# Kernel optimization log

Measured on AMD Instinct MI355X. Metric: run time of the kernel, lower is better.

## Reference

```python
import jax, jax.numpy as jnp
import numpy as np

NUM_HEADS = 8
LN_EPS = 1e-5


def setup_inputs() -> dict:
    key = jax.random.key(0)
    ks = jax.random.split(key, 8)
    B, C1, C2, H, W, D = 8, 384, 192, 16, 16, 16
    A = C1  # all_head_size = num_heads * (C1 // num_heads)
    s1, s2, sA = 1.0 / np.sqrt(C1), 1.0 / np.sqrt(C2), 1.0 / np.sqrt(A)
    return {
        "x1": jax.random.normal(ks[0], (B, C1, H, W, D), jnp.float32),
        "x2": jax.random.normal(ks[1], (B, C2, H, W, D), jnp.float32),
        "Wq": jax.random.normal(ks[2], (C1, A), jnp.float32) * s1,
        "bq": jnp.zeros((A,), jnp.float32),
        "Wk": jax.random.normal(ks[3], (C2, A), jnp.float32) * s2,
        "bk": jnp.zeros((A,), jnp.float32),
        "Wv": jax.random.normal(ks[4], (C2, A), jnp.float32) * s2,
        "bv": jnp.zeros((A,), jnp.float32),
        "Wo": jax.random.normal(ks[5], (A, C1), jnp.float32) * sA,
        "bo": jnp.zeros((C1,), jnp.float32),
        "gamma": jnp.ones((C1,), jnp.float32),
        "beta": jnp.zeros((C1,), jnp.float32),
    }


def reference(x1, x2, Wq, bq, Wk, bk, Wv, bv, Wo, bo, gamma, beta):
    B, C1, H, W, D = x1.shape
    L = H * W * D
    nh = NUM_HEADS
    dh = C1 // nh
    # flatten spatial dims to tokens: [B, L, C]
    x1f = x1.reshape(B, C1, L).transpose(0, 2, 1)
    x2f = x2.reshape(B, x2.shape[1], L).transpose(0, 2, 1)
    scale = dh ** 0.25
    q = (x1f @ Wq + bq).reshape(B, L, nh, dh) / scale  # [B,L,h,d]
    k = (x2f @ Wk + bk).reshape(B, L, nh, dh) / scale
    v = (x2f @ Wv + bv).reshape(B, L, nh, dh)
    # softmax over the token (L) axis of keys
    ksm = jax.nn.softmax(k, axis=1)
    # kernelized attention: KV outer product [B,h,d,e], then Q . KV
    kv = jnp.einsum('blhd,blhe->bhde', ksm, v)
    ctx = jnp.einsum('blhd,bhde->blhe', q, kv).reshape(B, L, nh * dh)
    out = ctx @ Wo + bo + x1f  # residual
    # LayerNorm over channel dim
    mu = out.mean(axis=-1, keepdims=True)
    var = out.var(axis=-1, keepdims=True)
    out = (out - mu) * jax.lax.rsqrt(var + LN_EPS) * gamma + beta
    return out.transpose(0, 2, 1).reshape(B, C1, H, W, D)
```

## Files before the change

kernel.cpp:

```cpp
#include <hip/hip_runtime.h>
#include <hip/hip_bf16.h>
#include <math.h>

#define BB 8
#define C1D 384
#define C2D 192
#define LDIM 4096
#define ADIM 384
#define NH 8
#define DHD 48
#define KVLC 16
#define KVP_STRIDE 2352
#define LN_EPS 1e-5f

typedef short s8v __attribute__((ext_vector_type(8)));
typedef float f4v __attribute__((ext_vector_type(4)));

__device__ __forceinline__ unsigned short f2bf(float f) {
    unsigned u = __builtin_bit_cast(unsigned, f);
    unsigned r = (u + 0x7FFFu + ((u >> 16) & 1u)) >> 16;
    return (unsigned short)r;
}
__device__ __forceinline__ float bf2f(unsigned short h) {
    unsigned u = ((unsigned)h) << 16;
    return __builtin_bit_cast(float, u);
}
__device__ __forceinline__ void gload16(const void* g, void* l) {
    __builtin_amdgcn_global_load_lds((const __attribute__((address_space(1))) void*)g,
                                     (__attribute__((address_space(3))) void*)l, 16, 0, 0);
}

__device__ __forceinline__ void tcvt_body(const float* __restrict__ ib,
                                          unsigned short* __restrict__ ob,
                                          int R, int Cols, int c0, int r0,
                                          float* smem, int t)
{
#pragma unroll
    for (int i = 0; i < 4; ++i) {
        int idx = t + i * 256;
        int rr = idx >> 5, cc = idx & 31;
        smem[rr * 33 + cc] = ib[(size_t)(r0 + rr) * Cols + c0 + cc];
    }
    __syncthreads();
#pragma unroll
    for (int i = 0; i < 2; ++i) {
        int idx = t + i * 256;
        int cc = idx >> 4, rp = (idx & 15) * 2;
        unsigned val = (unsigned)f2bf(smem[rp * 33 + cc]) | ((unsigned)f2bf(smem[(rp + 1) * 33 + cc]) << 16);
        *(unsigned*)&ob[(size_t)(c0 + cc) * R + r0 + rp] = val;
    }
}

__global__ __launch_bounds__(256) void pack_all(
    const float* __restrict__ x1, const float* __restrict__ x2,
    const float* __restrict__ Wk, const float* __restrict__ Wv, const float* __restrict__ Wo,
    const float* __restrict__ bk, const float* __restrict__ bv,
    unsigned short* __restrict__ X1p, unsigned short* __restrict__ X2p,
    unsigned short* __restrict__ Wkvp, unsigned short* __restrict__ WoTp,
    float* __restrict__ bkv)
{
    __shared__ float smem[32 * 33];
    int bid = blockIdx.x;
    int t = threadIdx.x;
    if (bid < 12288) {
        int i = bid;
        int c0 = (i % 128) * 32, r0 = ((i / 128) % 12) * 32, b = i / 1536;
        tcvt_body(x1 + (size_t)b * C1D * LDIM, X1p + (size_t)b * C1D * LDIM,
                  C1D, LDIM, c0, r0, smem, t);
    } else if (bid < 18432) {
        int i = bid - 12288;
        int c0 = (i % 128) * 32, r0 = ((i / 128) % 6) * 32, b = i / 768;
        tcvt_body(x2 + (size_t)b * C2D * LDIM, X2p + (size_t)b * C2D * LDIM,
                  C2D, LDIM, c0, r0, smem, t);
    } else if (bid < 18720) {
        int i = bid - 18432;
        if (i < 72)       tcvt_body(Wk, Wkvp,                      C2D,  ADIM, (i % 12) * 32, (i / 12) * 32, smem, t);
        else if (i < 144) { i -= 72;  tcvt_body(Wv, Wkvp + (size_t)ADIM * C2D, C2D, ADIM, (i % 12) * 32, (i / 12) * 32, smem, t); }
        else              { i -= 144; tcvt_body(Wo, WoTp,          ADIM, C1D,  (i % 12) * 32, (i / 12) * 32, smem, t); }
    } else {
        for (int i = t; i < 768; i += 256) bkv[i] = (i < 384) ? bk[i] : bv[i - 384];
    }
}

template<int KD, int BMODE>
__global__ __launch_bounds__(256) void gemm_mfma(
    const unsigned short* __restrict__ A, size_t Abs,
    const unsigned short* __restrict__ Bt, size_t Bbs,
    const float* __restrict__ bias,
    unsigned short* __restrict__ Out, size_t Obs, int Ncols,
    float scl, float scl2, int msplit, int gx, int gy)
{
    __shared__ unsigned short As[128 * 64];
    __shared__ unsigned short Bs[128 * 64];
    const int t = threadIdx.x;
    const int lane = t & 63;
    const int w = t >> 6;
    const int wm = w >> 1, wn = w & 1;
    const int nwg = gridDim.x;
    const int bid = blockIdx.x;
    const int swz = (bid & 7) * (nwg >> 3) + (bid >> 3);
    const int m0 = (swz % gx) * 128;
    const int n0 = ((swz / gx) % gy) * 128;
    const int b  = swz / (gx * gy);
    const float sEff = (m0 < msplit) ? scl : scl2;

    const unsigned short* Ab = A + Abs * b + (size_t)m0 * KD;
    const unsigned short* Bb = Bt + Bbs * b + (size_t)n0 * KD;

    f4v acc[4][4];
#pragma unroll
    for (int i = 0; i < 4; ++i)
#pragma unroll
        for (int j = 0; j < 4; ++j) acc[i][j] = (f4v)0.f;

    const int r_l = lane >> 3;
    const int q = lane & 7;

    for (int ks = 0; ks < KD; ks += 64) {
#pragma unroll
        for (int c = 0; c < 4; ++c) {
            int row = w * 32 + c * 8 + r_l;
            int koff = ((q ^ (row & 7)) << 3);
            gload16(Ab + (size_t)row * KD + ks + koff, &As[(w * 32 + c * 8) * 64]);
            gload16(Bb + (size_t)row * KD + ks + koff, &Bs[(w * 32 + c * 8) * 64]);
        }
        __syncthreads();
#pragma unroll
        for (int kh = 0; kh < 2; ++kh) {
            s8v af[4], bfr[4];
            int kq = kh * 4 + (lane >> 4);
#pragma unroll
            for (int m = 0; m < 4; ++m) {
                int row = wm * 64 + m * 16 + (lane & 15);
                af[m] = *(const s8v*)&As[row * 64 + ((kq ^ (row & 7)) << 3)];
            }
#pragma unroll
            for (int n = 0; n < 4; ++n) {
                int row = wn * 64 + n * 16 + (lane & 15);
                bfr[n] = *(const s8v*)&Bs[row * 64 + ((kq ^ (row & 7)) << 3)];
            }
#pragma unroll
            for (int m = 0; m < 4; ++m)
#pragma unroll
                for (int n = 0; n < 4; ++n)
                    acc[m][n] = __builtin_amdgcn_mfma_f32_16x16x32_bf16(af[m], bfr[n], acc[m][n], 0, 0, 0);
        }
        __syncthreads();
    }

    float bn[4], bm[4][4];
    if (BMODE == 2) {
#pragma unroll
        for (int m = 0; m < 4; ++m)
#pragma unroll
            for (int r = 0; r < 4; ++r)
                bm[m][r] = bias[m0 + wm * 64 + m * 16 + (lane >> 4) * 4 + r];
    } else if (BMODE == 1) {
#pragma unroll
        for (int n = 0; n < 4; ++n) bn[n] = bias[n0 + wn * 64 + n * 16 + (lane & 15)];
    }
#pragma unroll
    for (int m = 0; m < 4; ++m)
#pragma unroll
        for (int n = 0; n < 4; ++n) {
            int col = n0 + wn * 64 + n * 16 + (lane & 15);
#pragma unroll
            for (int r = 0; r < 4; ++r) {
                int row = m0 + wm * 64 + m * 16 + (lane >> 4) * 4 + r;
                float bb = (BMODE == 2) ? bm[m][r] : (BMODE == 1) ? bn[n] : 0.f;
                float v = (acc[m][n][r] + bb) * sEff;
                if (BMODE == 3 && row == col) v += 1.f;
                Out[Obs * b + (size_t)row * Ncols + col] = f2bf(v);
            }
        }
}

__global__ __launch_bounds__(64) void kv_part(const unsigned short* __restrict__ KVt,
                                              float* __restrict__ kvpart)
{
    int lane = threadIdx.x;
    int b = blockIdx.z, h = blockIdx.y, lc = blockIdx.x;
    size_t base = ((size_t)b * 768 + h * DHD) * LDIM;
    const unsigned short* Kb = KVt + base;
    const unsigned short* Vb = Kb + (size_t)ADIM * LDIM;
    int lbase = lc * (LDIM / KVLC);

    f4v acc[3][3];
#pragma unroll
    for (int i = 0; i < 3; ++i)
#pragma unroll
        for (int j = 0; j < 3; ++j) acc[i][j] = (f4v)0.f;
    float es[3] = {0.f, 0.f, 0.f};

    for (int ks = 0; ks < LDIM / KVLC; ks += 32) {
        int l0 = lbase + ks + ((lane >> 4) * 8);
        s8v af[3], bfr[3];
#pragma unroll
        for (int me = 0; me < 3; ++me)
            af[me] = *(const s8v*)&Vb[(size_t)(me * 16 + (lane & 15)) * LDIM + l0];
#pragma unroll
        for (int nd = 0; nd < 3; ++nd) {
            s8v raw = *(const s8v*)&Kb[(size_t)(nd * 16 + (lane & 15)) * LDIM + l0];
#pragma unroll
            for (int j = 0; j < 8; ++j) {
                float e = __expf(bf2f((unsigned short)raw[j]));
                es[nd] += e;
                bfr[nd][j] = (short)f2bf(e);
            }
        }
#pragma unroll
        for (int me = 0; me < 3; ++me)
#pragma unroll
            for (int nd = 0; nd < 3; ++nd)
                acc[me][nd] = __builtin_amdgcn_mfma_f32_16x16x32_bf16(af[me], bfr[nd], acc[me][nd], 0, 0, 0);
    }
    float* pp = kvpart + (((size_t)(b * NH + h) * KVLC) + lc) * KVP_STRIDE;
#pragma unroll
    for (int me = 0; me < 3; ++me)
#pragma unroll
        for (int nd = 0; nd < 3; ++nd)
#pragma unroll
            for (int r = 0; r < 4; ++r) {
                int e = me * 16 + (lane >> 4) * 4 + r;
                int d = nd * 16 + (lane & 15);
                pp[e * DHD + d] = acc[me][nd][r];
            }
#pragma unroll
    for (int nd = 0; nd < 3; ++nd) {
        float s = es[nd];
        s += __shfl_xor(s, 16, 64);
        s += __shfl_xor(s, 32, 64);
        if (lane < 16) pp[2304 + nd * 16 + lane] = s;
    }
}

__global__ __launch_bounds__(256) void kv_finalize(const float* __restrict__ kvpart,
                                                   float* __restrict__ KVf)
{
    __shared__ float isl_s[DHD];
    int bh = blockIdx.x, t = threadIdx.x;
    const float* pp = kvpart + (size_t)bh * KVLC * KVP_STRIDE;
    if (t < DHD) {
        float s = 0.f;
#pragma unroll
        for (int lc = 0; lc < KVLC; ++lc) s += pp[lc * KVP_STRIDE + 2304 + t];
        isl_s[t] = 1.f / s;
    }
    __syncthreads();
    for (int idx = t; idx < DHD * DHD; idx += 256) {
        int d = idx / DHD, e = idx % DHD;
        float s = 0.f;
#pragma unroll
        for (int lc = 0; lc < KVLC; ++lc) s += pp[lc * KVP_STRIDE + e * DHD + d];
        KVf[(size_t)bh * DHD * DHD + idx] = s * isl_s[d];
    }
}

__global__ __launch_bounds__(256) void mb_kernel(const float* __restrict__ Wq,
                                                 const float* __restrict__ bq,
                                                 const float* __restrict__ KVf,
                                                 const float* __restrict__ Wo,
                                                 const float* __restrict__ bo,
                                                 unsigned short* __restrict__ M,
                                                 float* __restrict__ btot, float inv_scale)
{
    __shared__ float smem[DHD * DHD];
    int blk = blockIdx.x, t = threadIdx.x;
    if (blk < 384) {
        int c0 = (blk % 6) * 64, h = (blk / 6) % 8, b = blk / 48;
        for (int idx = t; idx < DHD * DHD; idx += 256)
            smem[idx] = KVf[((size_t)(b * NH + h)) * DHD * DHD + idx];
        __syncthreads();
        int cl = t >> 2, qq = t & 3;
        int c = c0 + cl;
        float wq[DHD];
#pragma unroll
        for (int d = 0; d < DHD; ++d) wq[d] = Wq[(size_t)c * ADIM + h * DHD + d];
        float s[12];
#pragma unroll
        for (int j = 0; j < 12; ++j) s[j] = 0.f;
#pragma unroll
        for (int d = 0; d < DHD; ++d) {
            float w = wq[d];
#pragma unroll
            for (int j = 0; j < 12; ++j)
                s[j] += w * smem[d * DHD + qq * 12 + j];
        }
#pragma unroll
        for (int j = 0; j < 12; ++j)
            M[((size_t)b * C1D + c) * ADIM + h * DHD + qq * 12 + j] = f2bf(s[j] * inv_scale);
    } else {
        int k = blk - 384;
        int cp0 = (k % 12) * 32, b = k / 12;
        for (int idx = t; idx < ADIM; idx += 256) {
            int h = idx / DHD, e = idx % DHD;
            float s = 0.f;
#pragma unroll
            for (int d = 0; d < DHD; ++d)
                s += bq[h * DHD + d] * KVf[((size_t)(b * NH + h)) * DHD * DHD + d * DHD + e];
            smem[idx] = s * inv_scale;
        }
        __syncthreads();
        int cp = cp0 + (t >> 3), part = t & 7;
        float s = 0.f;
#pragma unroll
        for (int i = 0; i < 48; ++i) {
            int he = part * 48 + i;
            s += smem[he] * Wo[(size_t)he * C1D + cp];
        }
        s += __shfl_xor(s, 1, 64);
        s += __shfl_xor(s, 2, 64);
        s += __shfl_xor(s, 4, 64);
        if (part == 0) btot[b * C1D + cp] = s + bo[cp];
    }
}

__global__ __launch_bounds__(512) void gemm_lnT(
    const unsigned short* __restrict__ Wr,
    const unsigned short* __restrict__ Bx,
    const float* __restrict__ btot,
    const float* __restrict__ gamma,
    const float* __restrict__ beta,
    float* __restrict__ Y)
{
    __shared__ __align__(16) char lds[65536];
    unsigned short* As = (unsigned short*)lds;
    unsigned short* Bs = (unsigned short*)(lds + 49152);
    float* stats = (float*)lds;
    float* fin   = (float*)(lds + 8192);

    const int t = threadIdx.x;
    const int lane = t & 63;
    const int w = t >> 6;
    const int bid = blockIdx.x;
    const int swz = (bid & 7) * 32 + (bid >> 3);
    const int l0 = (swz & 31) * 128;
    const int b  = swz >> 5;

    const unsigned short* Ab = Wr + (size_t)b * C1D * C1D;
    const unsigned short* Bb = Bx + ((size_t)b * LDIM + l0) * C1D;

    f4v acc[3][8];
#pragma unroll
    for (int m = 0; m < 3; ++m)
#pragma unroll
        for (int n = 0; n < 8; ++n) acc[m][n] = (f4v)0.f;

    const int r_l = lane >> 3;
    const int q = lane & 7;

    for (int ks = 0; ks < C1D; ks += 64) {
#pragma unroll
        for (int c = 0; c < 6; ++c) {
            int row = w * 48 + c * 8 + r_l;
            int koff = ((q ^ (row & 7)) << 3);
            gload16(Ab + (size_t)row * C1D + ks + koff, &As[(w * 48 + c * 8) * 64]);
        }
#pragma unroll
        for (int c = 0; c < 2; ++c) {
            int row = w * 16 + c * 8 + r_l;
            int koff = ((q ^ (row & 7)) << 3);
            gload16(Bb + (size_t)row * C1D + ks + koff, &Bs[(w * 16 + c * 8) * 64]);
        }
        __syncthreads();
#pragma unroll
        for (int kh = 0; kh < 2; ++kh) {
            int kq = kh * 4 + (lane >> 4);
            s8v af[3], bfr[8];
#pragma unroll
            for (int m = 0; m < 3; ++m) {
                int row = w * 48 + m * 16 + (lane & 15);
                af[m] = *(const s8v*)&As[row * 64 + ((kq ^ (row & 7)) << 3)];
            }
#pragma unroll
            for (int n = 0; n < 8; ++n) {
                int row = n * 16 + (lane & 15);
                bfr[n] = *(const s8v*)&Bs[row * 64 + ((kq ^ (row & 7)) << 3)];
            }
#pragma unroll
            for (int m = 0; m < 3; ++m)
#pragma unroll
                for (int n = 0; n < 8; ++n)
                    acc[m][n] = __builtin_amdgcn_mfma_f32_16x16x32_bf16(af[m], bfr[n], acc[m][n], 0, 0, 0);
        }
        __syncthreads();
    }

    const int qq = lane >> 4;
    float btv[3][4], gmv[3][4], btav[3][4];
#pragma unroll
    for (int m = 0; m < 3; ++m)
#pragma unroll
        for (int r = 0; r < 4; ++r) {
            int row = w * 48 + m * 16 + qq * 4 + r;
            btv[m][r]  = btot[b * C1D + row];
            gmv[m][r]  = gamma[row];
            btav[m][r] = beta[row];
        }

    float cs[8], cq2[8];
#pragma unroll
    for (int n = 0; n < 8; ++n) { cs[n] = 0.f; cq2[n] = 0.f; }
#pragma unroll
    for (int m = 0; m < 3; ++m)
#pragma unroll
        for (int n = 0; n < 8; ++n)
#pragma unroll
            for (int r = 0; r < 4; ++r) {
                float v = acc[m][n][r] + btv[m][r];
                cs[n] += v; cq2[n] += v * v;
            }
#pragma unroll
    for (int n = 0; n < 8; ++n) {
        cs[n]  += __shfl_xor(cs[n], 16, 64);
        cs[n]  += __shfl_xor(cs[n], 32, 64);
        cq2[n] += __shfl_xor(cq2[n], 16, 64);
        cq2[n] += __shfl_xor(cq2[n], 32, 64);
    }
    if (lane < 16) {
#pragma unroll
        for (int n = 0; n < 8; ++n) {
            int col = n * 16 + lane;
            stats[(w * 128 + col) * 2 + 0] = cs[n];
            stats[(w * 128 + col) * 2 + 1] = cq2[n];
        }
    }
    __syncthreads();
    if (t < 256) {
        int col = t >> 1, which = t & 1;
        float s = 0.f;
#pragma unroll
        for (int w8 = 0; w8 < 8; ++w8) s += stats[(w8 * 128 + col) * 2 + which];
        fin[col * 2 + which] = s;
    }
    __syncthreads();

    float mu[8], rs[8];
#pragma unroll
    for (int n = 0; n < 8; ++n) {
        int cl = n * 16 + (lane & 15);
        float s = fin[cl * 2 + 0], s2 = fin[cl * 2 + 1];
        float m_ = s * (1.0f / C1D);
        mu[n] = m_;
        rs[n] = rsqrtf(s2 * (1.0f / C1D) - m_ * m_ + LN_EPS);
    }

    float* Yb = Y + (size_t)b * C1D * LDIM + l0;
#pragma unroll
    for (int m = 0; m < 3; ++m)
#pragma unroll
        for (int n = 0; n < 8; ++n)
#pragma unroll
            for (int r = 0; r < 4; ++r) {
                int row = w * 48 + m * 16 + qq * 4 + r;
                int cl = n * 16 + (lane & 15);
                float v = (acc[m][n][r] + btv[m][r] - mu[n]) * rs[n] * gmv[m][r] + btav[m][r];
                Yb[(size_t)row * LDIM + cl] = v;
            }
}

extern "C" void kernel_launch(void* const* d_in, const int* in_sizes, int n_in,
                              void* d_out, int out_size, void* d_ws, size_t ws_size,
                              hipStream_t stream) {
    const float* x1    = (const float*)d_in[0];
    const float* x2    = (const float*)d_in[1];
    const float* Wq    = (const float*)d_in[2];
    const float* bq    = (const float*)d_in[3];
    const float* Wk    = (const float*)d_in[4];
    const float* bk    = (const float*)d_in[5];
    const float* Wv    = (const float*)d_in[6];
    const float* bv    = (const float*)d_in[7];
    const float* Wo    = (const float*)d_in[8];
    const float* bo    = (const float*)d_in[9];
    const float* gamma = (const float*)d_in[10];
    const float* beta  = (const float*)d_in[11];
    float* out = (float*)d_out;

    char* p = (char*)d_ws;
    const size_t NB  = (size_t)BB * LDIM * ADIM;
    unsigned short* X1p = (unsigned short*)p; p += NB * 2;
    unsigned short* X2p = (unsigned short*)p; p += NB;
    unsigned short* KVt = (unsigned short*)p; p += (size_t)BB * 768 * LDIM * 2;
    unsigned short* Wkvp= (unsigned short*)p; p += (size_t)768 * C2D * 2;
    unsigned short* WoTp= (unsigned short*)p; p += (size_t)C1D * ADIM * 2;
    float* bkv    = (float*)p; p += 768 * 4;
    float* kvpart = (float*)p; p += (size_t)BB * NH * KVLC * KVP_STRIDE * 4;
    float* KVf    = (float*)p; p += (size_t)BB * NH * DHD * DHD * 4;
    unsigned short* Mbuf = (unsigned short*)p; p += (size_t)BB * C1D * ADIM * 2;
    unsigned short* WresT = (unsigned short*)p; p += (size_t)BB * C1D * C1D * 2;
    float* btot   = (float*)p; p += (size_t)BB * C1D * 4;

    float inv_scale = powf((float)DHD, -0.25f);

    pack_all<<<18721, 256, 0, stream>>>(x1, x2, Wk, Wv, Wo, bk, bv, X1p, X2p, Wkvp, WoTp, bkv);

    gemm_mfma<C2D, 2><<<1536, 256, 0, stream>>>(
        Wkvp, 0, X2p, (size_t)LDIM * C2D, bkv, KVt, (size_t)768 * LDIM, LDIM,
        inv_scale, 1.0f, ADIM, 6, 32);

    kv_part<<<dim3(KVLC, NH, BB), 64, 0, stream>>>(KVt, kvpart);
    kv_finalize<<<BB * NH, 256, 0, stream>>>(kvpart, KVf);

    mb_kernel<<<480, 256, 0, stream>>>(Wq, bq, KVf, Wo, bo, Mbuf, btot, inv_scale);

    gemm_mfma<ADIM, 3><<<72, 256, 0, stream>>>(
        WoTp, 0, Mbuf, (size_t)C1D * ADIM, bo , WresT, (size_t)C1D * C1D, C1D,
        1.0f, 1.0f, 1 << 30, 3, 3);

    gemm_lnT<<<256, 512, 0, stream>>>(WresT, X1p, btot, gamma, beta, out);
}
```

Measured before the change: 117.6 us.

## Fuse K/V projection GEMM with exp and KV partial reduction in one kernel

Replaces the separate K/V projection GEMM, which wrote a full bf16 KVt intermediate to global memory, and the kv_part kernel with a single kv_fused kernel. Each block computes the K and V projections for one head and a 256-token chunk in LDS, applies bias, scaling and exp to K, then does the KV outer-product MFMA and the per-chunk exp sums directly. The Wk/Wv packing is interleaved per head so one A tile covers both K and V for a head. This removes a large global write and reread, at the cost of a bigger LDS footprint and 512-thread blocks, with only 9 of the 8 waves' worth of MFMA tiles in the second stage.

```diff
diff --git a/kernel.cpp b/kernel.cpp
--- a/kernel.cpp
+++ b/kernel.cpp
@@ -33,7 +33,7 @@
 __device__ __forceinline__ void tcvt_body(const float* __restrict__ ib,
                                           unsigned short* __restrict__ ob,
                                           int R, int Cols, int c0, int r0,
-                                          float* smem, int t)
+                                          float* smem, int t, int rmode)
 {
 #pragma unroll
     for (int i = 0; i < 4; ++i) {
@@ -47,17 +47,17 @@
         int idx = t + i * 256;
         int cc = idx >> 4, rp = (idx & 15) * 2;
         unsigned val = (unsigned)f2bf(smem[rp * 33 + cc]) | ((unsigned)f2bf(smem[(rp + 1) * 33 + cc]) << 16);
-        *(unsigned*)&ob[(size_t)(c0 + cc) * R + r0 + rp] = val;
+        int a = c0 + cc;
+        int orow = (rmode == 0) ? a : ((a / 48) * 96 + (a % 48) + ((rmode == 2) ? 48 : 0));
+        *(unsigned*)&ob[(size_t)orow * R + r0 + rp] = val;
     }
 }
 
 __global__ __launch_bounds__(256) void pack_all(
     const float* __restrict__ x1, const float* __restrict__ x2,
     const float* __restrict__ Wk, const float* __restrict__ Wv, const float* __restrict__ Wo,
-    const float* __restrict__ bk, const float* __restrict__ bv,
     unsigned short* __restrict__ X1p, unsigned short* __restrict__ X2p,
-    unsigned short* __restrict__ Wkvp, unsigned short* __restrict__ WoTp,
-    float* __restrict__ bkv)
+    unsigned short* __restrict__ Wkvp, unsigned short* __restrict__ WoTp)
 {
     __shared__ float smem[32 * 33];
     int bid = blockIdx.x;
@@ -66,19 +66,17 @@
         int i = bid;
         int c0 = (i % 128) * 32, r0 = ((i / 128) % 12) * 32, b = i / 1536;
         tcvt_body(x1 + (size_t)b * C1D * LDIM, X1p + (size_t)b * C1D * LDIM,
-                  C1D, LDIM, c0, r0, smem, t);
+                  C1D, LDIM, c0, r0, smem, t, 0);
     } else if (bid < 18432) {
         int i = bid - 12288;
         int c0 = (i % 128) * 32, r0 = ((i / 128) % 6) * 32, b = i / 768;
         tcvt_body(x2 + (size_t)b * C2D * LDIM, X2p + (size_t)b * C2D * LDIM,
-                  C2D, LDIM, c0, r0, smem, t);
-    } else if (bid < 18720) {
+                  C2D, LDIM, c0, r0, smem, t, 0);
+    } else {
         int i = bid - 18432;
-        if (i < 72)       tcvt_body(Wk, Wkvp,                      C2D,  ADIM, (i % 12) * 32, (i / 12) * 32, smem, t);
-        else if (i < 144) { i -= 72;  tcvt_body(Wv, Wkvp + (size_t)ADIM * C2D, C2D, ADIM, (i % 12) * 32, (i / 12) * 32, smem, t); }
-        else              { i -= 144; tcvt_body(Wo, WoTp,          ADIM, C1D,  (i % 12) * 32, (i / 12) * 32, smem, t); }
-    } else {
-        for (int i = t; i < 768; i += 256) bkv[i] = (i < 384) ? bk[i] : bv[i - 384];
+        if (i < 72)       tcvt_body(Wk, Wkvp, C2D,  ADIM, (i % 12) * 32, (i / 12) * 32, smem, t, 1);
+        else if (i < 144) { i -= 72;  tcvt_body(Wv, Wkvp, C2D, ADIM, (i % 12) * 32, (i / 12) * 32, smem, t, 2); }
+        else              { i -= 144; tcvt_body(Wo, WoTp, ADIM, C1D,  (i % 12) * 32, (i / 12) * 32, smem, t, 0); }
     }
 }
 
@@ -86,9 +84,7 @@
 __global__ __launch_bounds__(256) void gemm_mfma(
     const unsigned short* __restrict__ A, size_t Abs,
     const unsigned short* __restrict__ Bt, size_t Bbs,
-    const float* __restrict__ bias,
-    unsigned short* __restrict__ Out, size_t Obs, int Ncols,
-    float scl, float scl2, int msplit, int gx, int gy)
+    unsigned short* __restrict__ Out, size_t Obs, int Ncols, int gx, int gy)
 {
     __shared__ unsigned short As[128 * 64];
     __shared__ unsigned short Bs[128 * 64];
@@ -102,7 +98,6 @@
     const int m0 = (swz % gx) * 128;
     const int n0 = ((swz / gx) % gy) * 128;
     const int b  = swz / (gx * gy);
-    const float sEff = (m0 < msplit) ? scl : scl2;
 
     const unsigned short* Ab = A + Abs * b + (size_t)m0 * KD;
     const unsigned short* Bb = Bt + Bbs * b + (size_t)n0 * KD;
@@ -148,17 +143,6 @@
         __syncthreads();
     }
 
-    float bn[4], bm[4][4];
-    if (BMODE == 2) {
-#pragma unroll
-        for (int m = 0; m < 4; ++m)
-#pragma unroll
-            for (int r = 0; r < 4; ++r)
-                bm[m][r] = bias[m0 + wm * 64 + m * 16 + (lane >> 4) * 4 + r];
-    } else if (BMODE == 1) {
-#pragma unroll
-        for (int n = 0; n < 4; ++n) bn[n] = bias[n0 + wn * 64 + n * 16 + (lane & 15)];
-    }
 #pragma unroll
     for (int m = 0; m < 4; ++m)
 #pragma unroll
@@ -167,70 +151,142 @@
 #pragma unroll
             for (int r = 0; r < 4; ++r) {
                 int row = m0 + wm * 64 + m * 16 + (lane >> 4) * 4 + r;
-                float bb = (BMODE == 2) ? bm[m][r] : (BMODE == 1) ? bn[n] : 0.f;
-                float v = (acc[m][n][r] + bb) * sEff;
+                float v = acc[m][n][r];
                 if (BMODE == 3 && row == col) v += 1.f;
                 Out[Obs * b + (size_t)row * Ncols + col] = f2bf(v);
             }
         }
 }
 
-__global__ __launch_bounds__(64) void kv_part(const unsigned short* __restrict__ KVt,
-                                              float* __restrict__ kvpart)
-{
-    int lane = threadIdx.x;
-    int b = blockIdx.z, h = blockIdx.y, lc = blockIdx.x;
-    size_t base = ((size_t)b * 768 + h * DHD) * LDIM;
-    const unsigned short* Kb = KVt + base;
-    const unsigned short* Vb = Kb + (size_t)ADIM * LDIM;
-    int lbase = lc * (LDIM / KVLC);
-
-    f4v acc[3][3];
-#pragma unroll
-    for (int i = 0; i < 3; ++i)
-#pragma unroll
-        for (int j = 0; j < 3; ++j) acc[i][j] = (f4v)0.f;
-    float es[3] = {0.f, 0.f, 0.f};
-
-    for (int ks = 0; ks < LDIM / KVLC; ks += 32) {
-        int l0 = lbase + ks + ((lane >> 4) * 8);
-        s8v af[3], bfr[3];
-#pragma unroll
-        for (int me = 0; me < 3; ++me)
-            af[me] = *(const s8v*)&Vb[(size_t)(me * 16 + (lane & 15)) * LDIM + l0];
-#pragma unroll
-        for (int nd = 0; nd < 3; ++nd) {
-            s8v raw = *(const s8v*)&Kb[(size_t)(nd * 16 + (lane & 15)) * LDIM + l0];
-#pragma unroll
-            for (int j = 0; j < 8; ++j) {
-                float e = __expf(bf2f((unsigned short)raw[j]));
-                es[nd] += e;
-                bfr[nd][j] = (short)f2bf(e);
-            }
-        }
-#pragma unroll
-        for (int me = 0; me < 3; ++me)
-#pragma unroll
-            for (int nd = 0; nd < 3; ++nd)
-                acc[me][nd] = __builtin_amdgcn_mfma_f32_16x16x32_bf16(af[me], bfr[nd], acc[me][nd], 0, 0, 0);
-    }
-    float* pp = kvpart + (((size_t)(b * NH + h) * KVLC) + lc) * KVP_STRIDE;
-#pragma unroll
-    for (int me = 0; me < 3; ++me)
-#pragma unroll
-        for (int nd = 0; nd < 3; ++nd)
+__global__ __launch_bounds__(512) void kv_fused(
+    const unsigned short* __restrict__ Wkvp,
+    const unsigned short* __restrict__ X2p,
+    const float* __restrict__ bk, const float* __restrict__ bv,
+    float* __restrict__ kvpart, float inv_scale)
+{
+    __shared__ __align__(16) char lds[50176];
+    unsigned short* As = (unsigned short*)lds;
+    unsigned short* Bs = (unsigned short*)(lds + 12288);
+    unsigned short* Ks = (unsigned short*)lds;
+    unsigned short* Vs = (unsigned short*)(lds + 24576);
+    float* exps = (float*)(lds + 49152);
+
+    const int t = threadIdx.x, lane = t & 63, w = t >> 6;
+    const int wm = w >> 2, wn = w & 3;
+    const int r_l = lane >> 3, q = lane & 7, qq = lane >> 4;
+    const int bid = blockIdx.x;
+    const int swz = (bid & 7) * 128 + (bid >> 3);
+    const int lc = swz & 15, h = (swz >> 4) & 7, b = swz >> 7;
+
+    const unsigned short* Ab = Wkvp + (size_t)h * 96 * C2D;
+    const unsigned short* Bb = X2p + ((size_t)b * LDIM + lc * 256) * C2D;
+
+    f4v acc[3][4];
+#pragma unroll
+    for (int m = 0; m < 3; ++m)
+#pragma unroll
+        for (int n = 0; n < 4; ++n) acc[m][n] = (f4v)0.f;
+
+    for (int ks = 0; ks < C2D; ks += 64) {
+#pragma unroll
+        for (int c = 0; c < 2; ++c) {
+            int blk = w + c * 8;
+            if (blk < 12) {
+                int row = blk * 8 + r_l;
+                gload16(Ab + (size_t)row * C2D + ks + ((q ^ r_l) << 3), &As[blk * 8 * 64]);
+            }
+        }
+#pragma unroll
+        for (int c = 0; c < 4; ++c) {
+            int blk = w * 4 + c;
+            int row = blk * 8 + r_l;
+            gload16(Bb + (size_t)row * C2D + ks + ((q ^ r_l) << 3), &Bs[blk * 8 * 64]);
+        }
+        __syncthreads();
+#pragma unroll
+        for (int kh = 0; kh < 2; ++kh) {
+            int kq = kh * 4 + qq;
+            s8v af[3], bfr[4];
+#pragma unroll
+            for (int m = 0; m < 3; ++m) {
+                int row = wm * 48 + m * 16 + (lane & 15);
+                af[m] = *(const s8v*)&As[row * 64 + ((kq ^ (row & 7)) << 3)];
+            }
+#pragma unroll
+            for (int n = 0; n < 4; ++n) {
+                int row = wn * 64 + n * 16 + (lane & 15);
+                bfr[n] = *(const s8v*)&Bs[row * 64 + ((kq ^ (row & 7)) << 3)];
+            }
+#pragma unroll
+            for (int m = 0; m < 3; ++m)
+#pragma unroll
+                for (int n = 0; n < 4; ++n)
+                    acc[m][n] = __builtin_amdgcn_mfma_f32_16x16x32_bf16(af[m], bfr[n], acc[m][n], 0, 0, 0);
+        }
+        __syncthreads();
+    }
+
+    float es[3][4];
+#pragma unroll
+    for (int m = 0; m < 3; ++m)
+#pragma unroll
+        for (int r = 0; r < 4; ++r) es[m][r] = 0.f;
+
+#pragma unroll
+    for (int m = 0; m < 3; ++m)
+#pragma unroll
+        for (int r = 0; r < 4; ++r) {
+            int rr = m * 16 + qq * 4 + r;
+            float bias = (wm == 0) ? bk[h * DHD + rr] : bv[h * DHD + rr];
+#pragma unroll
+            for (int n = 0; n < 4; ++n) {
+                int col = wn * 64 + n * 16 + (lane & 15);
+                float v = acc[m][n][r] + bias;
+                if (wm == 0) {
+                    float e = __expf(v * inv_scale);
+                    es[m][r] += e;
+                    *(unsigned short*)((char*)Ks + rr * 512 + ((col * 2) ^ ((rr & 7) << 4))) = f2bf(e);
+                } else {
+                    *(unsigned short*)((char*)Vs + rr * 512 + ((col * 2) ^ ((rr & 7) << 4))) = f2bf(v);
+                }
+            }
+        }
+    if (wm == 0) {
+#pragma unroll
+        for (int m = 0; m < 3; ++m)
 #pragma unroll
             for (int r = 0; r < 4; ++r) {
-                int e = me * 16 + (lane >> 4) * 4 + r;
-                int d = nd * 16 + (lane & 15);
-                pp[e * DHD + d] = acc[me][nd][r];
-            }
-#pragma unroll
-    for (int nd = 0; nd < 3; ++nd) {
-        float s = es[nd];
-        s += __shfl_xor(s, 16, 64);
-        s += __shfl_xor(s, 32, 64);
-        if (lane < 16) pp[2304 + nd * 16 + lane] = s;
+                float s = es[m][r];
+                s += __shfl_xor(s, 1, 64);
+                s += __shfl_xor(s, 2, 64);
+                s += __shfl_xor(s, 4, 64);
+                s += __shfl_xor(s, 8, 64);
+                if ((lane & 15) == 0) exps[(m * 16 + qq * 4 + r) * 4 + wn] = s;
+            }
+    }
+    __syncthreads();
+
+    float* pp = kvpart + ((size_t)(b * NH + h) * KVLC + lc) * KVP_STRIDE;
+    if (t < 48) pp[2304 + t] = exps[t * 4 + 0] + exps[t * 4 + 1] + exps[t * 4 + 2] + exps[t * 4 + 3];
+
+    for (int fi = w; fi < 9; fi += 8) {
+        int me = fi / 3, nd = fi % 3;
+        f4v a2 = (f4v)0.f;
+#pragma unroll
+        for (int kc = 0; kc < 8; ++kc) {
+            int k0 = kc * 32 + qq * 8;
+            int e = me * 16 + (lane & 15);
+            int d = nd * 16 + (lane & 15);
+            s8v av = *(const s8v*)((char*)Vs + e * 512 + ((k0 * 2) ^ ((e & 7) << 4)));
+            s8v bk_ = *(const s8v*)((char*)Ks + d * 512 + ((k0 * 2) ^ ((d & 7) << 4)));
+            a2 = __builtin_amdgcn_mfma_f32_16x16x32_bf16(av, bk_, a2, 0, 0, 0);
+        }
+#pragma unroll
+        for (int r = 0; r < 4; ++r) {
+            int e = me * 16 + qq * 4 + r;
+            int d = nd * 16 + (lane & 15);
+            pp[e * DHD + d] = a2[r];
+        }
     }
 }
 
@@ -480,10 +536,8 @@
     const size_t NB  = (size_t)BB * LDIM * ADIM;
     unsigned short* X1p = (unsigned short*)p; p += NB * 2;
     unsigned short* X2p = (unsigned short*)p; p += NB;
-    unsigned short* KVt = (unsigned short*)p; p += (size_t)BB * 768 * LDIM * 2;
     unsigned short* Wkvp= (unsigned short*)p; p += (size_t)768 * C2D * 2;
     unsigned short* WoTp= (unsigned short*)p; p += (size_t)C1D * ADIM * 2;
-    float* bkv    = (float*)p; p += 768 * 4;
     float* kvpart = (float*)p; p += (size_t)BB * NH * KVLC * KVP_STRIDE * 4;
     float* KVf    = (float*)p; p += (size_t)BB * NH * DHD * DHD * 4;
     unsigned short* Mbuf = (unsigned short*)p; p += (size_t)BB * C1D * ADIM * 2;
@@ -492,20 +546,16 @@
 
     float inv_scale = powf((float)DHD, -0.25f);
 
-    pack_all<<<18721, 256, 0, stream>>>(x1, x2, Wk, Wv, Wo, bk, bv, X1p, X2p, Wkvp, WoTp, bkv);
-
-    gemm_mfma<C2D, 2><<<1536, 256, 0, stream>>>(
-        Wkvp, 0, X2p, (size_t)LDIM * C2D, bkv, KVt, (size_t)768 * LDIM, LDIM,
-        inv_scale, 1.0f, ADIM, 6, 32);
-
-    kv_part<<<dim3(KVLC, NH, BB), 64, 0, stream>>>(KVt, kvpart);
+    pack_all<<<18720, 256, 0, stream>>>(x1, x2, Wk, Wv, Wo, X1p, X2p, Wkvp, WoTp);
+
+    kv_fused<<<1024, 512, 0, stream>>>(Wkvp, X2p, bk, bv, kvpart, inv_scale);
+
     kv_finalize<<<BB * NH, 256, 0, stream>>>(kvpart, KVf);
 
     mb_kernel<<<480, 256, 0, stream>>>(Wq, bq, KVf, Wo, bo, Mbuf, btot, inv_scale);
 
     gemm_mfma<ADIM, 3><<<72, 256, 0, stream>>>(
-        WoTp, 0, Mbuf, (size_t)C1D * ADIM, bo , WresT, (size_t)C1D * C1D, C1D,
-        1.0f, 1.0f, 1 << 30, 3, 3);
+        WoTp, 0, Mbuf, (size_t)C1D * ADIM, WresT, (size_t)C1D * C1D, C1D, 3, 3);
 
     gemm_lnT<<<256, 512, 0, stream>>>(WresT, X1p, btot, gamma, beta, out);
 }
```

Measured after the change: 105.7 us (median of 2 runs). 10.2% less time.
